# Kernel tuning notes

Measured on AMD Instinct MI355X. Metric: run time of the kernel, lower is better.

Reference implementation:

```python
import jax, jax.numpy as jnp
import numpy as np

B, NIN, D = 2048, 64, 128
N_LCB, N_FMB, RANK = 32, 32, 24
DIM_HIDDEN = 1024
N_OUT = N_LCB + N_FMB  # == NIN -> identity residual
MAX_VAL = 1.0
EPS_LN_FMB_MIN, EPS_LN_FMB_MAX = 1e-11, 1e7
KERAS_LN_EPS = 1e-3


def setup_inputs() -> dict:
    key = jax.random.key(0)
    ks = jax.random.split(key, 9)
    def w(k, shape, fan):
        return (jax.random.normal(k, shape, jnp.float32) / np.sqrt(fan)).astype(jnp.float32)
    return {
        "x": jax.random.normal(ks[0], (B, NIN, D), jnp.float32),
        "noise": jax.random.uniform(ks[1], (B, N_OUT, D), jnp.float32),
        "w_lcb": w(ks[2], (NIN, N_LCB), NIN),
        "w_rank": w(ks[3], (NIN, RANK), NIN),
        "w1": w(ks[4], (NIN * RANK, DIM_HIDDEN), NIN * RANK),
        "w2": w(ks[5], (DIM_HIDDEN, DIM_HIDDEN), DIM_HIDDEN),
        "w3": w(ks[6], (DIM_HIDDEN, N_FMB * D), DIM_HIDDEN),
        "gamma": jnp.ones((D,), jnp.float32),
        "beta": jnp.zeros((D,), jnp.float32),
    }


def _forward(x, noise, w_lcb, w_rank, w1, w2, w3, gamma, beta):
    # ---- LinearCompressBlock: Dense over feature (emb-count) axis ----
    lcb = jnp.einsum("bnd,nm->bmd", x, w_lcb)  # (B, N_LCB, D)

    # ---- FactorizationMachineBlock ----
    # rank_layer on transposed input: (B, D, NIN) @ (NIN, RANK)
    r = jnp.einsum("bnd,nr->bdr", x, w_rank)          # (B, D, RANK)
    fm = jnp.einsum("bnd,bdr->bnr", x, r)             # (B, NIN, RANK)
    fm = fm.reshape(fm.shape[0], NIN * RANK)
    # custom LayerNorm (no affine, clipped std)
    mu = jnp.mean(fm, axis=-1, keepdims=True)
    cen = fm - mu
    std = jnp.sqrt(jnp.mean(cen * cen, axis=-1, keepdims=True))
    std = jnp.clip(std, EPS_LN_FMB_MIN, EPS_LN_FMB_MAX)
    fm = cen / std
    # MLP: 2 hidden relu layers + linear out, dropout=0 / inference
    h = jax.nn.relu(fm @ w1)
    h = jax.nn.relu(h @ w2)
    fmb = (h @ w3).reshape(-1, N_FMB, D)              # (B, N_FMB, D)

    out = jnp.concatenate((fmb, lcb), axis=1)          # (B, N_OUT, D)
    residual = x                                        # NIN == N_OUT -> identity

    safe = jnp.clip(out, -MAX_VAL, MAX_VAL)
    a = jnp.abs(safe)
    c = lambda t: jnp.clip(t, -MAX_VAL, MAX_VAL)

    # conv term: reshape to (B, N, D//8, 8), 1x1 conv with all-ones (8->8)
    # filter == group-sum broadcast back over the 8 lanes
    g = safe.reshape(safe.shape[0], N_OUT, D // 8, 8)
    conv = jnp.broadcast_to(g.sum(-1, keepdims=True), g.shape).reshape(safe.shape)

    extra = (
        c(jnp.log(a + 1.0))
        + c(jax.lax.rsqrt(a + 1.0))
        + c(jax.nn.softmax(safe, axis=-1))
        + c(jnp.tanh(safe))
        + c(jnp.where(safe >= 0, safe, 0.2 * safe))          # leaky_relu alpha=0.2
        + c(jnp.exp(safe))
        + c(jax.nn.softplus(safe))
        + c(jnp.log1p(a))
        + jnp.zeros_like(safe)                               # zeros_like term
        + c(jnp.round(safe))
        + jnp.ones_like(safe)                                # pow(a+eps, 0) == 1
        + c(jnp.sign(safe))
        + c(jnp.prod(safe, axis=-1, keepdims=True))
        + c(jnp.isnan(safe).astype(jnp.float32))
        + c((~(safe < 0)).astype(jnp.float32))
        + c((safe != 0).astype(jnp.float32))
        + c((safe >= 0).astype(jnp.float32))
        + c(safe.astype(jnp.int8).astype(jnp.float32))       # bitwise_and(x,x)==x after int8 cast
        + c(jnp.max(safe, axis=-1, keepdims=True))
        + c(safe + safe)                                     # add_n([safe, safe])
        + c(safe + safe)                                     # raw Add
        + 7.0 * safe                                         # slice/split-concat/merge/einsum/squeeze/pad/stack identities (|safe|<=1 so clip no-op)
        + c(jnp.where(safe > 0.5, -1.0, safe))               # tensor_scatter_nd_update
        + c(conv)
        + c(noise)                                           # tf.random.uniform (deterministic input)
        + c(jnp.arange(D, dtype=jnp.float32))                # broadcast over last axis
        + c(jnp.sum(safe[0] * safe[0], axis=-1))[None, :, None]  # DiagPart(matmul(safe[0], safe[0]^T))
    )

    pre = out + residual + 1e-10 * extra
    # keras LayerNormalization(axis=-1), default epsilon=1e-3
    m = jnp.mean(pre, axis=-1, keepdims=True)
    v = jnp.mean(jnp.square(pre - m), axis=-1, keepdims=True)
    return (pre - m) * jax.lax.rsqrt(v + KERAS_LN_EPS) * gamma + beta


def reference(x, noise, w_lcb, w_rank, w1, w2, w3, gamma, beta):
    return _forward(x, noise, w_lcb, w_rank, w1, w2, w3, gamma, beta)
```

## Files before the change

### kernel.cpp

```cpp
#include <hip/hip_runtime.h>


typedef _Float16 half8_t __attribute__((ext_vector_type(8)));
typedef _Float16 half4_t __attribute__((ext_vector_type(4)));
typedef float floatx4 __attribute__((ext_vector_type(4)));

#define B_SZ 2048
#define NIN 64
#define D_SZ 128
#define RANK 24
#define FMK (NIN * RANK)
#define HID 1024
#define NFMB_D (32 * 128)

__global__ __launch_bounds__(256) void transpose_cast(
    const float* __restrict__ w, _Float16* __restrict__ wt, int K, int N) {
  __shared__ float tile[32][33];
  const int tk = blockIdx.x * 32;
  const int tn = blockIdx.y * 32;
  const int tx = threadIdx.x & 31;
  const int ty = threadIdx.x >> 5;
#pragma unroll
  for (int i = 0; i < 4; i++) {
    int k = ty + i * 8;
    tile[k][tx] = w[(size_t)(tk + k) * N + (tn + tx)];
  }
  __syncthreads();
#pragma unroll
  for (int i = 0; i < 4; i++) {
    int n = ty + i * 8;
    wt[(size_t)(tn + n) * K + (tk + tx)] = (_Float16)tile[tx][n];
  }
}

#define STX 72
#define STN 136
__global__ __launch_bounds__(256, 2) void front_kernel(
    const float* __restrict__ x, const float* __restrict__ w_rank,
    const float* __restrict__ w_lcb, _Float16* __restrict__ fmn,
    _Float16* __restrict__ lcb16) {
  constexpr int XT_OFF = 0;
  constexpr int X16_OFF = 18432;
  constexpr int RT_OFF = X16_OFF + 17408;
  constexpr int WRT_OFF = RT_OFF + 8704;
  constexpr int WLT_OFF = WRT_OFF + 4608;
  constexpr int RED_OFF = WLT_OFF + 4608;
  __shared__ __align__(16) char smem[RED_OFF + 32];
  _Float16* xT = (_Float16*)(smem + XT_OFF);
  _Float16* x16 = (_Float16*)(smem + X16_OFF);
  _Float16* rT = (_Float16*)(smem + RT_OFF);
  _Float16* wrT = (_Float16*)(smem + WRT_OFF);
  _Float16* wlT = (_Float16*)(smem + WLT_OFF);
  float* redbuf = (float*)(smem + RED_OFF);
  _Float16* lcb_s = (_Float16*)(smem + X16_OFF);
  _Float16* fmn_s = (_Float16*)(smem + RT_OFF);

  const int b = blockIdx.x, t = threadIdx.x;
  const int lane = t & 63;
  const int w = __builtin_amdgcn_readfirstlane(t >> 6);
  const int q = lane >> 4, ln = lane & 15;

  const float4* xg4 = (const float4*)(x + (size_t)b * (NIN * D_SZ));
#pragma unroll
  for (int hh = 0; hh < 2; hh++) {
    int bb = t + hh * 256;
    int n0 = (bb >> 5) * 4;
    int bd = bb & 31;
    int d0 = bd * 4;
    float4 L0 = xg4[(n0 + 0) * 32 + bd];
    float4 L1 = xg4[(n0 + 1) * 32 + bd];
    float4 L2 = xg4[(n0 + 2) * 32 + bd];
    float4 L3 = xg4[(n0 + 3) * 32 + bd];
    *(half4_t*)&x16[(n0 + 0) * STN + d0] =
        half4_t{(_Float16)L0.x, (_Float16)L0.y, (_Float16)L0.z, (_Float16)L0.w};
    *(half4_t*)&x16[(n0 + 1) * STN + d0] =
        half4_t{(_Float16)L1.x, (_Float16)L1.y, (_Float16)L1.z, (_Float16)L1.w};
    *(half4_t*)&x16[(n0 + 2) * STN + d0] =
        half4_t{(_Float16)L2.x, (_Float16)L2.y, (_Float16)L2.z, (_Float16)L2.w};
    *(half4_t*)&x16[(n0 + 3) * STN + d0] =
        half4_t{(_Float16)L3.x, (_Float16)L3.y, (_Float16)L3.z, (_Float16)L3.w};
    *(half4_t*)&xT[(d0 + 0) * STX + n0] =
        half4_t{(_Float16)L0.x, (_Float16)L1.x, (_Float16)L2.x, (_Float16)L3.x};
    *(half4_t*)&xT[(d0 + 1) * STX + n0] =
        half4_t{(_Float16)L0.y, (_Float16)L1.y, (_Float16)L2.y, (_Float16)L3.y};
    *(half4_t*)&xT[(d0 + 2) * STX + n0] =
        half4_t{(_Float16)L0.z, (_Float16)L1.z, (_Float16)L2.z, (_Float16)L3.z};
    *(half4_t*)&xT[(d0 + 3) * STX + n0] =
        half4_t{(_Float16)L0.w, (_Float16)L1.w, (_Float16)L2.w, (_Float16)L3.w};
  }
#pragma unroll
  for (int k = 0; k < 6; k++) {
    int i = t + k * 256;
    int n = i / 24, j = i - n * 24;
    wrT[j * STX + n] = (_Float16)w_rank[i];
  }
#pragma unroll
  for (int k = 0; k < 2; k++) {
    int i = t + k * 256;
    wrT[(24 + (i >> 6)) * STX + (i & 63)] = (_Float16)0.f;
  }
#pragma unroll
  for (int k = 0; k < 8; k++) {
    int i = t + k * 256;
    wlT[(i & 31) * STX + (i >> 5)] = (_Float16)w_lcb[i];
  }
  __syncthreads();

  floatx4 r_acc[2][2] = {};
  floatx4 l_acc[2][2] = {};
#pragma unroll
  for (int k = 0; k < 2; k++) {
    half8_t bfrag[2], ar[2], al[2];
#pragma unroll
    for (int ni = 0; ni < 2; ni++)
      bfrag[ni] =
          *(const half8_t*)&xT[((2 * w + ni) * 16 + ln) * STX + k * 32 + q * 8];
#pragma unroll
    for (int mi = 0; mi < 2; mi++) {
      ar[mi] = *(const half8_t*)&wrT[(mi * 16 + ln) * STX + k * 32 + q * 8];
      al[mi] = *(const half8_t*)&wlT[(mi * 16 + ln) * STX + k * 32 + q * 8];
    }
#pragma unroll
    for (int mi = 0; mi < 2; mi++)
#pragma unroll
      for (int ni = 0; ni < 2; ni++) {
        r_acc[mi][ni] = __builtin_amdgcn_mfma_f32_16x16x32_f16(
            ar[mi], bfrag[ni], r_acc[mi][ni], 0, 0, 0);
        l_acc[mi][ni] = __builtin_amdgcn_mfma_f32_16x16x32_f16(
            al[mi], bfrag[ni], l_acc[mi][ni], 0, 0, 0);
      }
  }
#pragma unroll
  for (int mi = 0; mi < 2; mi++)
#pragma unroll
    for (int ni = 0; ni < 2; ni++)
#pragma unroll
      for (int rr = 0; rr < 4; rr++)
        rT[(mi * 16 + q * 4 + rr) * STN + (2 * w + ni) * 16 + ln] =
            (_Float16)r_acc[mi][ni][rr];
  __syncthreads();

  floatx4 f_acc[2] = {};
#pragma unroll
  for (int k = 0; k < 4; k++) {
    half8_t af = *(const half8_t*)&x16[(w * 16 + ln) * STN + k * 32 + q * 8];
#pragma unroll
    for (int nj = 0; nj < 2; nj++) {
      half8_t bf = *(const half8_t*)&rT[(nj * 16 + ln) * STN + k * 32 + q * 8];
      f_acc[nj] =
          __builtin_amdgcn_mfma_f32_16x16x32_f16(af, bf, f_acc[nj], 0, 0, 0);
    }
  }
  float s = 0.f, s2 = 0.f;
#pragma unroll
  for (int rr = 0; rr < 4; rr++) {
    float v = f_acc[0][rr];
    s += v;
    s2 += v * v;
    float v1 = (ln < 8) ? f_acc[1][rr] : 0.f;
    s += v1;
    s2 += v1 * v1;
  }
#pragma unroll
  for (int off = 1; off < 64; off <<= 1) {
    s += __shfl_xor(s, off);
    s2 += __shfl_xor(s2, off);
  }
  if (lane == 0) {
    redbuf[w * 2] = s;
    redbuf[w * 2 + 1] = s2;
  }
  __syncthreads();
  s = redbuf[0] + redbuf[2] + redbuf[4] + redbuf[6];
  s2 = redbuf[1] + redbuf[3] + redbuf[5] + redbuf[7];
  const float mu = s * (1.f / FMK);
  float var = s2 * (1.f / FMK) - mu * mu;
  var = var > 0.f ? var : 0.f;
  float sd = sqrtf(var);
  sd = sd < 1e-11f ? 1e-11f : (sd > 1e7f ? 1e7f : sd);
  const float inv = 1.f / sd;

#pragma unroll
  for (int nj = 0; nj < 2; nj++) {
    int j = nj * 16 + ln;
    if (j < RANK) {
#pragma unroll
      for (int rr = 0; rr < 4; rr++)
        fmn_s[(w * 16 + q * 4 + rr) * RANK + j] =
            (_Float16)((f_acc[nj][rr] - mu) * inv);
    }
  }
#pragma unroll
  for (int mi = 0; mi < 2; mi++)
#pragma unroll
    for (int ni = 0; ni < 2; ni++)
#pragma unroll
      for (int rr = 0; rr < 4; rr++)
        lcb_s[(mi * 16 + q * 4 + rr) * 128 + (2 * w + ni) * 16 + ln] =
            (_Float16)l_acc[mi][ni][rr];
  __syncthreads();
  half8_t* fg = (half8_t*)(fmn + (size_t)b * FMK);
  if (t < FMK / 8) fg[t] = ((const half8_t*)fmn_s)[t];
  half8_t* lg = (half8_t*)(lcb16 + (size_t)b * NFMB_D);
#pragma unroll
  for (int i = 0; i < 2; i++)
    lg[t + i * 256] = ((const half8_t*)lcb_s)[t + i * 256];
}

template <int MT, bool RELU>
__global__ __launch_bounds__(256, 2) void gemm_bt(
    const _Float16* __restrict__ A, const _Float16* __restrict__ Bt,
    _Float16* __restrict__ C, int M, int N, int K) {
  constexpr int LDT = 40;
  constexpr int MI = MT / 32;
  __shared__ __align__(16) _Float16 As[MT * LDT];
  __shared__ __align__(16) _Float16 Bs[128 * LDT];
  const int m0 = blockIdx.x * MT;
  const int n0 = blockIdx.y * 128;
  const int t = threadIdx.x;
  const int wave = t >> 6, lane = t & 63;
  const int wr = wave >> 1, wc = wave & 1;
  const int q = lane >> 4, ln = lane & 15;
  const int srow = t >> 2;
  const int skc = t & 3;
  const _Float16* gA0 = A + (size_t)(m0 + srow) * K + skc * 8;
  const _Float16* gA1 = gA0 + (size_t)64 * K;
  const _Float16* gB0 = Bt + (size_t)(n0 + srow) * K + skc * 8;
  const _Float16* gB1 = gB0 + (size_t)64 * K;
  const int ldsw = srow * LDT + skc * 8;

  floatx4 acc[MI][4] = {};

  uint4 ra0 = *(const uint4*)(gA0);
  uint4 ra1;
  if constexpr (MT == 128) ra1 = *(const uint4*)(gA1);
  uint4 rb0 = *(const uint4*)(gB0);
  uint4 rb1 = *(const uint4*)(gB1);

  for (int k0 = 0;;) {
    __syncthreads();
    *(uint4*)&As[ldsw] = ra0;
    if constexpr (MT == 128) *(uint4*)&As[64 * LDT + ldsw] = ra1;
    *(uint4*)&Bs[ldsw] = rb0;
    *(uint4*)&Bs[64 * LDT + ldsw] = rb1;
    __syncthreads();
    k0 += 32;
    if (k0 < K) {
      ra0 = *(const uint4*)(gA0 + k0);
      if constexpr (MT == 128) ra1 = *(const uint4*)(gA1 + k0);
      rb0 = *(const uint4*)(gB0 + k0);
      rb1 = *(const uint4*)(gB1 + k0);
    }
    half8_t af[MI], bf[4];
#pragma unroll
    for (int i = 0; i < MI; i++)
      af[i] = *(const half8_t*)&As[(wr * (MT / 2) + i * 16 + ln) * LDT + q * 8];
#pragma unroll
    for (int j = 0; j < 4; j++)
      bf[j] = *(const half8_t*)&Bs[(wc * 64 + j * 16 + ln) * LDT + q * 8];
#pragma unroll
    for (int i = 0; i < MI; i++)
#pragma unroll
      for (int j = 0; j < 4; j++)
        acc[i][j] =
            __builtin_amdgcn_mfma_f32_16x16x32_f16(af[i], bf[j], acc[i][j], 0, 0, 0);
    if (k0 >= K) break;
  }

#pragma unroll
  for (int i = 0; i < MI; i++) {
#pragma unroll
    for (int r = 0; r < 4; r++) {
      size_t row = (size_t)(m0 + wr * (MT / 2) + i * 16 + q * 4 + r);
      _Float16* crow = C + row * N + n0 + wc * 64 + ln;
#pragma unroll
      for (int j = 0; j < 4; j++) {
        float v = acc[i][j][r];
        if (RELU) v = v > 0.f ? v : 0.f;
        crow[j * 16] = (_Float16)v;
      }
    }
  }
}

__global__ __launch_bounds__(256) void epilogue_kernel(
    const float* __restrict__ x, const _Float16* __restrict__ fmb,
    const _Float16* __restrict__ lcb16, const float* __restrict__ gamma,
    const float* __restrict__ beta, float* __restrict__ out) {
  __shared__ __align__(16) _Float16 pre[NIN * D_SZ];
  __shared__ float mrow[64], rrow[64];
  const int b = blockIdx.x, t = threadIdx.x;
  const float4* xb4 = (const float4*)(x + (size_t)b * (NIN * D_SZ));
  const half8_t* fb8 = (const half8_t*)(fmb + (size_t)b * NFMB_D);
  const half8_t* lb8 = (const half8_t*)(lcb16 + (size_t)b * NFMB_D);
#pragma unroll
  for (int ii = 0; ii < 4; ii++) {
    int g = t + ii * 256;
    half8_t p = (g < 512) ? fb8[g] : lb8[g - 512];
    float4 xa = xb4[g * 2], xc = xb4[g * 2 + 1];
    half8_t o;
    o[0] = (_Float16)((float)p[0] + xa.x);
    o[1] = (_Float16)((float)p[1] + xa.y);
    o[2] = (_Float16)((float)p[2] + xa.z);
    o[3] = (_Float16)((float)p[3] + xa.w);
    o[4] = (_Float16)((float)p[4] + xc.x);
    o[5] = (_Float16)((float)p[5] + xc.y);
    o[6] = (_Float16)((float)p[6] + xc.z);
    o[7] = (_Float16)((float)p[7] + xc.w);
    *(half8_t*)&pre[g * 8] = o;
  }
  __syncthreads();
  {
    const int c = t >> 2, qd = t & 3;
    float s = 0.f, s2 = 0.f;
    const _Float16* pr = pre + c * 128 + qd * 32;
    for (int k = 0; k < 32; k++) {
      float v = (float)pr[(k + t) & 31];
      s += v;
      s2 += v * v;
    }
    s += __shfl_xor(s, 1);
    s2 += __shfl_xor(s2, 1);
    s += __shfl_xor(s, 2);
    s2 += __shfl_xor(s2, 2);
    if (qd == 0) {
      float m = s * (1.f / 128.f);
      float var = s2 * (1.f / 128.f) - m * m;
      mrow[c] = m;
      rrow[c] = rsqrtf(var + 1e-3f);
    }
  }
  __syncthreads();
  float4* ob4 = (float4*)(out + (size_t)b * (NIN * D_SZ));
  const float4* g4 = (const float4*)gamma;
  const float4* be4 = (const float4*)beta;
#pragma unroll
  for (int ii = 0; ii < 4; ii++) {
    int i8 = t + ii * 256;
    int c = i8 >> 4;
    int d8 = i8 & 15;
    float m = mrow[c], rstd = rrow[c];
    half8_t p = *(const half8_t*)&pre[i8 * 8];
    float4 g0 = g4[d8 * 2], g1 = g4[d8 * 2 + 1];
    float4 b0 = be4[d8 * 2], b1 = be4[d8 * 2 + 1];
    float4 o0, o1;
    o0.x = ((float)p[0] - m) * rstd * g0.x + b0.x;
    o0.y = ((float)p[1] - m) * rstd * g0.y + b0.y;
    o0.z = ((float)p[2] - m) * rstd * g0.z + b0.z;
    o0.w = ((float)p[3] - m) * rstd * g0.w + b0.w;
    o1.x = ((float)p[4] - m) * rstd * g1.x + b1.x;
    o1.y = ((float)p[5] - m) * rstd * g1.y + b1.y;
    o1.z = ((float)p[6] - m) * rstd * g1.z + b1.z;
    o1.w = ((float)p[7] - m) * rstd * g1.w + b1.w;
    ob4[i8 * 2] = o0;
    ob4[i8 * 2 + 1] = o1;
  }
}

extern "C" void kernel_launch(void* const* d_in, const int* in_sizes, int n_in,
                              void* d_out, int out_size, void* d_ws,
                              size_t ws_size, hipStream_t stream) {
  const float* x = (const float*)d_in[0];
  const float* w_lcb = (const float*)d_in[2];
  const float* w_rank = (const float*)d_in[3];
  const float* w1 = (const float*)d_in[4];
  const float* w2 = (const float*)d_in[5];
  const float* w3 = (const float*)d_in[6];
  const float* gamma = (const float*)d_in[7];
  const float* beta = (const float*)d_in[8];
  float* out = (float*)d_out;

  char* ws = (char*)d_ws;
  _Float16* w1t = (_Float16*)ws; ws += (size_t)HID * FMK * 2;
  _Float16* w2t = (_Float16*)ws; ws += (size_t)HID * HID * 2;
  _Float16* w3t = (_Float16*)ws; ws += (size_t)NFMB_D * HID * 2;
  _Float16* fmn = (_Float16*)ws; ws += (size_t)B_SZ * FMK * 2;
  _Float16* h1  = (_Float16*)ws; ws += (size_t)B_SZ * HID * 2;
  _Float16* fmb = (_Float16*)ws; ws += (size_t)B_SZ * NFMB_D * 2;
  _Float16* lcb16 = (_Float16*)ws; ws += (size_t)B_SZ * NFMB_D * 2;
  _Float16* h2 = fmn;

  transpose_cast<<<dim3(FMK / 32, HID / 32), 256, 0, stream>>>(w1, w1t, FMK, HID);
  transpose_cast<<<dim3(HID / 32, HID / 32), 256, 0, stream>>>(w2, w2t, HID, HID);
  transpose_cast<<<dim3(HID / 32, NFMB_D / 32), 256, 0, stream>>>(w3, w3t, HID, NFMB_D);
  front_kernel<<<B_SZ, 256, 0, stream>>>(x, w_rank, w_lcb, fmn, lcb16);
  gemm_bt<64, true><<<dim3(B_SZ / 64, HID / 128), 256, 0, stream>>>(fmn, w1t, h1, B_SZ, HID, FMK);
  gemm_bt<64, true><<<dim3(B_SZ / 64, HID / 128), 256, 0, stream>>>(h1, w2t, h2, B_SZ, HID, HID);
  gemm_bt<128, false><<<dim3(B_SZ / 128, NFMB_D / 128), 256, 0, stream>>>(h2, w3t, fmb, B_SZ, NFMB_D, HID);
  epilogue_kernel<<<B_SZ, 256, 0, stream>>>(x, fmb, lcb16, gamma, beta, out);
}
```

Baseline: 277.4 us.

## Fuse final layernorm into w3 GEMM and front kernel, merge weight transposes

The separate epilogue kernel goes away. The w3 GEMM now adds the residual and applies the per-row layernorm directly on its 128x128 output tile, since each tile covers exactly one feature row of 128. The LCB half is normalized inside the front kernel. This removes the fp16 round trips of fmb and lcb16 through global memory, plus one launch. The three weight transpose launches are also merged into one. The residual add is now done in fp32 accumulators rather than after fp16 rounding of the GEMM output. The GEMM adds extra shared memory for the x tile, which may lower occupancy.

```diff
diff --git a/kernel.cpp b/kernel.cpp
--- a/kernel.cpp
+++ b/kernel.cpp
@@ -12,12 +12,28 @@
 #define FMK (NIN * RANK)
 #define HID 1024
 #define NFMB_D (32 * 128)
-
-__global__ __launch_bounds__(256) void transpose_cast(
-    const float* __restrict__ w, _Float16* __restrict__ wt, int K, int N) {
+#define ROW_F (NIN * D_SZ)
+
+__global__ __launch_bounds__(256) void transpose_cast_all(
+    const float* __restrict__ w1, const float* __restrict__ w2,
+    const float* __restrict__ w3, _Float16* __restrict__ w1t,
+    _Float16* __restrict__ w2t, _Float16* __restrict__ w3t) {
   __shared__ float tile[32][33];
-  const int tk = blockIdx.x * 32;
-  const int tn = blockIdx.y * 32;
+  int bid = blockIdx.x;
+  const float* w;
+  _Float16* wt;
+  int K, N, kt;
+  if (bid < 48 * 32) {
+    w = w1; wt = w1t; K = FMK; N = HID; kt = 48;
+  } else if (bid < 48 * 32 + 32 * 32) {
+    bid -= 48 * 32;
+    w = w2; wt = w2t; K = HID; N = HID; kt = 32;
+  } else {
+    bid -= 48 * 32 + 32 * 32;
+    w = w3; wt = w3t; K = HID; N = NFMB_D; kt = 32;
+  }
+  const int tk = (bid % kt) * 32;
+  const int tn = (bid / kt) * 32;
   const int tx = threadIdx.x & 31;
   const int ty = threadIdx.x >> 5;
 #pragma unroll
@@ -37,8 +53,9 @@
 #define STN 136
 __global__ __launch_bounds__(256, 2) void front_kernel(
     const float* __restrict__ x, const float* __restrict__ w_rank,
-    const float* __restrict__ w_lcb, _Float16* __restrict__ fmn,
-    _Float16* __restrict__ lcb16) {
+    const float* __restrict__ w_lcb, const float* __restrict__ gamma,
+    const float* __restrict__ beta, _Float16* __restrict__ fmn,
+    float* __restrict__ out) {
   constexpr int XT_OFF = 0;
   constexpr int X16_OFF = 18432;
   constexpr int RT_OFF = X16_OFF + 17408;
@@ -46,13 +63,13 @@
   constexpr int WLT_OFF = WRT_OFF + 4608;
   constexpr int RED_OFF = WLT_OFF + 4608;
   __shared__ __align__(16) char smem[RED_OFF + 32];
+  __shared__ float2 lstat[32][4];
   _Float16* xT = (_Float16*)(smem + XT_OFF);
   _Float16* x16 = (_Float16*)(smem + X16_OFF);
   _Float16* rT = (_Float16*)(smem + RT_OFF);
   _Float16* wrT = (_Float16*)(smem + WRT_OFF);
   _Float16* wlT = (_Float16*)(smem + WLT_OFF);
   float* redbuf = (float*)(smem + RED_OFF);
-  _Float16* lcb_s = (_Float16*)(smem + X16_OFF);
   _Float16* fmn_s = (_Float16*)(smem + RT_OFF);
 
   const int b = blockIdx.x, t = threadIdx.x;
@@ -60,7 +77,7 @@
   const int w = __builtin_amdgcn_readfirstlane(t >> 6);
   const int q = lane >> 4, ln = lane & 15;
 
-  const float4* xg4 = (const float4*)(x + (size_t)b * (NIN * D_SZ));
+  const float4* xg4 = (const float4*)(x + (size_t)b * ROW_F);
 #pragma unroll
   for (int hh = 0; hh < 2; hh++) {
     int bb = t + hh * 256;
@@ -190,21 +207,62 @@
             (_Float16)((f_acc[nj][rr] - mu) * inv);
     }
   }
+
+  const int d0 = (2 * w) * 16 + ln;
+  const int d1 = d0 + 16;
+  const float g0 = gamma[d0], g1 = gamma[d1];
+  const float be0 = beta[d0], be1 = beta[d1];
+  float lv0[2][4], lv1[2][4];
+  float sw[2][4], s2w[2][4];
 #pragma unroll
   for (int mi = 0; mi < 2; mi++)
 #pragma unroll
-    for (int ni = 0; ni < 2; ni++)
+    for (int rr = 0; rr < 4; rr++) {
+      int m = mi * 16 + q * 4 + rr;
+      float v0 = l_acc[mi][0][rr] + (float)x16[(32 + m) * STN + d0];
+      float v1 = l_acc[mi][1][rr] + (float)x16[(32 + m) * STN + d1];
+      lv0[mi][rr] = v0;
+      lv1[mi][rr] = v1;
+      sw[mi][rr] = v0 + v1;
+      s2w[mi][rr] = v0 * v0 + v1 * v1;
+    }
+#pragma unroll
+  for (int off = 1; off < 16; off <<= 1) {
+#pragma unroll
+    for (int mi = 0; mi < 2; mi++)
+#pragma unroll
+      for (int rr = 0; rr < 4; rr++) {
+        sw[mi][rr] += __shfl_xor(sw[mi][rr], off);
+        s2w[mi][rr] += __shfl_xor(s2w[mi][rr], off);
+      }
+  }
+  if (ln == 0) {
+#pragma unroll
+    for (int mi = 0; mi < 2; mi++)
 #pragma unroll
       for (int rr = 0; rr < 4; rr++)
-        lcb_s[(mi * 16 + q * 4 + rr) * 128 + (2 * w + ni) * 16 + ln] =
-            (_Float16)l_acc[mi][ni][rr];
-  __syncthreads();
+        lstat[mi * 16 + q * 4 + rr][w] = float2{sw[mi][rr], s2w[mi][rr]};
+  }
+  __syncthreads();
+
   half8_t* fg = (half8_t*)(fmn + (size_t)b * FMK);
   if (t < FMK / 8) fg[t] = ((const half8_t*)fmn_s)[t];
-  half8_t* lg = (half8_t*)(lcb16 + (size_t)b * NFMB_D);
-#pragma unroll
-  for (int i = 0; i < 2; i++)
-    lg[t + i * 256] = ((const half8_t*)lcb_s)[t + i * 256];
+  float* ob = out + (size_t)b * ROW_F;
+#pragma unroll
+  for (int mi = 0; mi < 2; mi++)
+#pragma unroll
+    for (int rr = 0; rr < 4; rr++) {
+      int m = mi * 16 + q * 4 + rr;
+      float2 p0 = lstat[m][0], p1 = lstat[m][1];
+      float2 p2 = lstat[m][2], p3 = lstat[m][3];
+      float S = p0.x + p1.x + p2.x + p3.x;
+      float S2 = p0.y + p1.y + p2.y + p3.y;
+      float mean = S * (1.f / 128.f);
+      float varr = S2 * (1.f / 128.f) - mean * mean;
+      float rstd = rsqrtf(varr + 1e-3f);
+      ob[(32 + m) * 128 + d0] = (lv0[mi][rr] - mean) * rstd * g0 + be0;
+      ob[(32 + m) * 128 + d1] = (lv1[mi][rr] - mean) * rstd * g1 + be1;
+    }
 }
 
 template <int MT, bool RELU>
@@ -283,78 +341,133 @@
   }
 }
 
-__global__ __launch_bounds__(256) void epilogue_kernel(
-    const float* __restrict__ x, const _Float16* __restrict__ fmb,
-    const _Float16* __restrict__ lcb16, const float* __restrict__ gamma,
+__global__ __launch_bounds__(256, 2) void gemm_ln(
+    const _Float16* __restrict__ A, const _Float16* __restrict__ Bt,
+    const float* __restrict__ x, const float* __restrict__ gamma,
     const float* __restrict__ beta, float* __restrict__ out) {
-  __shared__ __align__(16) _Float16 pre[NIN * D_SZ];
-  __shared__ float mrow[64], rrow[64];
-  const int b = blockIdx.x, t = threadIdx.x;
-  const float4* xb4 = (const float4*)(x + (size_t)b * (NIN * D_SZ));
-  const half8_t* fb8 = (const half8_t*)(fmb + (size_t)b * NFMB_D);
-  const half8_t* lb8 = (const half8_t*)(lcb16 + (size_t)b * NFMB_D);
-#pragma unroll
-  for (int ii = 0; ii < 4; ii++) {
-    int g = t + ii * 256;
-    half8_t p = (g < 512) ? fb8[g] : lb8[g - 512];
-    float4 xa = xb4[g * 2], xc = xb4[g * 2 + 1];
-    half8_t o;
-    o[0] = (_Float16)((float)p[0] + xa.x);
-    o[1] = (_Float16)((float)p[1] + xa.y);
-    o[2] = (_Float16)((float)p[2] + xa.z);
-    o[3] = (_Float16)((float)p[3] + xa.w);
-    o[4] = (_Float16)((float)p[4] + xc.x);
-    o[5] = (_Float16)((float)p[5] + xc.y);
-    o[6] = (_Float16)((float)p[6] + xc.z);
-    o[7] = (_Float16)((float)p[7] + xc.w);
-    *(half8_t*)&pre[g * 8] = o;
-  }
-  __syncthreads();
-  {
-    const int c = t >> 2, qd = t & 3;
-    float s = 0.f, s2 = 0.f;
-    const _Float16* pr = pre + c * 128 + qd * 32;
-    for (int k = 0; k < 32; k++) {
-      float v = (float)pr[(k + t) & 31];
-      s += v;
-      s2 += v * v;
-    }
-    s += __shfl_xor(s, 1);
-    s2 += __shfl_xor(s2, 1);
-    s += __shfl_xor(s, 2);
-    s2 += __shfl_xor(s2, 2);
-    if (qd == 0) {
-      float m = s * (1.f / 128.f);
-      float var = s2 * (1.f / 128.f) - m * m;
-      mrow[c] = m;
-      rrow[c] = rsqrtf(var + 1e-3f);
-    }
-  }
-  __syncthreads();
-  float4* ob4 = (float4*)(out + (size_t)b * (NIN * D_SZ));
-  const float4* g4 = (const float4*)gamma;
-  const float4* be4 = (const float4*)beta;
-#pragma unroll
-  for (int ii = 0; ii < 4; ii++) {
-    int i8 = t + ii * 256;
-    int c = i8 >> 4;
-    int d8 = i8 & 15;
-    float m = mrow[c], rstd = rrow[c];
-    half8_t p = *(const half8_t*)&pre[i8 * 8];
-    float4 g0 = g4[d8 * 2], g1 = g4[d8 * 2 + 1];
-    float4 b0 = be4[d8 * 2], b1 = be4[d8 * 2 + 1];
-    float4 o0, o1;
-    o0.x = ((float)p[0] - m) * rstd * g0.x + b0.x;
-    o0.y = ((float)p[1] - m) * rstd * g0.y + b0.y;
-    o0.z = ((float)p[2] - m) * rstd * g0.z + b0.z;
-    o0.w = ((float)p[3] - m) * rstd * g0.w + b0.w;
-    o1.x = ((float)p[4] - m) * rstd * g1.x + b1.x;
-    o1.y = ((float)p[5] - m) * rstd * g1.y + b1.y;
-    o1.z = ((float)p[6] - m) * rstd * g1.z + b1.z;
-    o1.w = ((float)p[7] - m) * rstd * g1.w + b1.w;
-    ob4[i8 * 2] = o0;
-    ob4[i8 * 2 + 1] = o1;
-  }
+  constexpr int LDT = 40;
+  constexpr int LDXS = 132;
+  constexpr int K = HID;
+  __shared__ __align__(16) _Float16 As[128 * LDT];
+  __shared__ __align__(16) _Float16 Bs[128 * LDT];
+  __shared__ __align__(16) _Float16 xs[128 * LDXS];
+  __shared__ float2 rowst[128][2];
+  const int m0 = blockIdx.x * 128;
+  const int c = blockIdx.y;
+  const int n0 = c * 128;
+  const int t = threadIdx.x;
+  const int wave = t >> 6, lane = t & 63;
+  const int wr = wave >> 1, wc = wave & 1;
+  const int q = lane >> 4, ln = lane & 15;
+  const int srow = t >> 2;
+  const int skc = t & 3;
+  const _Float16* gA0 = A + (size_t)(m0 + srow) * K + skc * 8;
+  const _Float16* gA1 = gA0 + (size_t)64 * K;
+  const _Float16* gB0 = Bt + (size_t)(n0 + srow) * K + skc * 8;
+  const _Float16* gB1 = gB0 + (size_t)64 * K;
+  const int ldsw = srow * LDT + skc * 8;
+
+  floatx4 acc[4][4] = {};
+  uint4 ra0 = *(const uint4*)(gA0);
+  uint4 ra1 = *(const uint4*)(gA1);
+  uint4 rb0 = *(const uint4*)(gB0);
+  uint4 rb1 = *(const uint4*)(gB1);
+
+  for (int k0 = 0;;) {
+    __syncthreads();
+    *(uint4*)&As[ldsw] = ra0;
+    *(uint4*)&As[64 * LDT + ldsw] = ra1;
+    *(uint4*)&Bs[ldsw] = rb0;
+    *(uint4*)&Bs[64 * LDT + ldsw] = rb1;
+    __syncthreads();
+    k0 += 32;
+    if (k0 < K) {
+      ra0 = *(const uint4*)(gA0 + k0);
+      ra1 = *(const uint4*)(gA1 + k0);
+      rb0 = *(const uint4*)(gB0 + k0);
+      rb1 = *(const uint4*)(gB1 + k0);
+    }
+    half8_t af[4], bf[4];
+#pragma unroll
+    for (int i = 0; i < 4; i++)
+      af[i] = *(const half8_t*)&As[(wr * 64 + i * 16 + ln) * LDT + q * 8];
+#pragma unroll
+    for (int j = 0; j < 4; j++)
+      bf[j] = *(const half8_t*)&Bs[(wc * 64 + j * 16 + ln) * LDT + q * 8];
+#pragma unroll
+    for (int i = 0; i < 4; i++)
+#pragma unroll
+      for (int j = 0; j < 4; j++)
+        acc[i][j] =
+            __builtin_amdgcn_mfma_f32_16x16x32_f16(af[i], bf[j], acc[i][j], 0, 0, 0);
+    if (k0 >= K) break;
+  }
+
+#pragma unroll
+  for (int ii = 0; ii < 16; ii++) {
+    int idx = t + ii * 256;
+    int row = idx >> 5, f4 = idx & 31;
+    float4 v = *(const float4*)(x + (size_t)(m0 + row) * ROW_F + n0 + f4 * 4);
+    *(half4_t*)&xs[row * LDXS + f4 * 4] =
+        half4_t{(_Float16)v.x, (_Float16)v.y, (_Float16)v.z, (_Float16)v.w};
+  }
+  __syncthreads();
+
+  float s[4][4], s2[4][4];
+#pragma unroll
+  for (int i = 0; i < 4; i++)
+#pragma unroll
+    for (int r = 0; r < 4; r++) {
+      int row = wr * 64 + i * 16 + q * 4 + r;
+      float ss = 0.f, qq = 0.f;
+#pragma unroll
+      for (int j = 0; j < 4; j++) {
+        float v = acc[i][j][r] + (float)xs[row * LDXS + wc * 64 + j * 16 + ln];
+        acc[i][j][r] = v;
+        ss += v;
+        qq += v * v;
+      }
+      s[i][r] = ss;
+      s2[i][r] = qq;
+    }
+#pragma unroll
+  for (int off = 1; off < 16; off <<= 1) {
+#pragma unroll
+    for (int i = 0; i < 4; i++)
+#pragma unroll
+      for (int r = 0; r < 4; r++) {
+        s[i][r] += __shfl_xor(s[i][r], off);
+        s2[i][r] += __shfl_xor(s2[i][r], off);
+      }
+  }
+  if (ln == 0) {
+#pragma unroll
+    for (int i = 0; i < 4; i++)
+#pragma unroll
+      for (int r = 0; r < 4; r++)
+        rowst[wr * 64 + i * 16 + q * 4 + r][wc] = float2{s[i][r], s2[i][r]};
+  }
+  __syncthreads();
+  float g[4], bb[4];
+#pragma unroll
+  for (int j = 0; j < 4; j++) {
+    g[j] = gamma[wc * 64 + j * 16 + ln];
+    bb[j] = beta[wc * 64 + j * 16 + ln];
+  }
+#pragma unroll
+  for (int i = 0; i < 4; i++)
+#pragma unroll
+    for (int r = 0; r < 4; r++) {
+      int row = wr * 64 + i * 16 + q * 4 + r;
+      float2 p0 = rowst[row][0], p1 = rowst[row][1];
+      float mean = (p0.x + p1.x) * (1.f / 128.f);
+      float varr = (p0.y + p1.y) * (1.f / 128.f) - mean * mean;
+      float rstd = rsqrtf(varr + 1e-3f);
+      float* orow = out + (size_t)(m0 + row) * ROW_F + n0 + wc * 64 + ln;
+#pragma unroll
+      for (int j = 0; j < 4; j++)
+        orow[j * 16] = (acc[i][j][r] - mean) * rstd * g[j] + bb[j];
+    }
 }
 
 extern "C" void kernel_launch(void* const* d_in, const int* in_sizes, int n_in,
@@ -376,16 +489,14 @@
   _Float16* w3t = (_Float16*)ws; ws += (size_t)NFMB_D * HID * 2;
   _Float16* fmn = (_Float16*)ws; ws += (size_t)B_SZ * FMK * 2;
   _Float16* h1  = (_Float16*)ws; ws += (size_t)B_SZ * HID * 2;
-  _Float16* fmb = (_Float16*)ws; ws += (size_t)B_SZ * NFMB_D * 2;
-  _Float16* lcb16 = (_Float16*)ws; ws += (size_t)B_SZ * NFMB_D * 2;
   _Float16* h2 = fmn;
 
-  transpose_cast<<<dim3(FMK / 32, HID / 32), 256, 0, stream>>>(w1, w1t, FMK, HID);
-  transpose_cast<<<dim3(HID / 32, HID / 32), 256, 0, stream>>>(w2, w2t, HID, HID);
-  transpose_cast<<<dim3(HID / 32, NFMB_D / 32), 256, 0, stream>>>(w3, w3t, HID, NFMB_D);
-  front_kernel<<<B_SZ, 256, 0, stream>>>(x, w_rank, w_lcb, fmn, lcb16);
-  gemm_bt<64, true><<<dim3(B_SZ / 64, HID / 128), 256, 0, stream>>>(fmn, w1t, h1, B_SZ, HID, FMK);
-  gemm_bt<64, true><<<dim3(B_SZ / 64, HID / 128), 256, 0, stream>>>(h1, w2t, h2, B_SZ, HID, HID);
-  gemm_bt<128, false><<<dim3(B_SZ / 128, NFMB_D / 128), 256, 0, stream>>>(h2, w3t, fmb, B_SZ, NFMB_D, HID);
-  epilogue_kernel<<<B_SZ, 256, 0, stream>>>(x, fmb, lcb16, gamma, beta, out);
+  transpose_cast_all<<<48 * 32 + 32 * 32 + 32 * 128, 256, 0, stream>>>(
+      w1, w2, w3, w1t, w2t, w3t);
+  front_kernel<<<B_SZ, 256, 0, stream>>>(x, w_rank, w_lcb, gamma, beta, fmn, out);
+  gemm_bt<64, true><<<dim3(B_SZ / 64, HID / 128), 256, 0, stream>>>(
+      fmn, w1t, h1, B_SZ, HID, FMK);
+  gemm_bt<64, true><<<dim3(B_SZ / 64, HID / 128), 256, 0, stream>>>(
+      h1, w2t, h2, B_SZ, HID, HID);
+  gemm_ln<<<dim3(B_SZ / 128, 32), 256, 0, stream>>>(h2, w3t, x, gamma, beta, out);
 }
```

New measurement: 263.0 us. 5.2% less time.
